# Optimization experiments

Measured on AMD Instinct MI355X. Metric: run time of the kernel, lower is better.

Reference implementation:

```python
import jax, jax.numpy as jnp
import numpy as np
from jax import lax

B, T = 64, 2048
RNN_DIM, EMB_DIM, ATT_DIM = 1024, 512, 128
N_FILT, KSIZE = 32, 31
PAD = (KSIZE - 1) // 2


def setup_inputs() -> dict:
    key = jax.random.key(0)
    ks = jax.random.split(key, 9)
    return {
        "query": jax.random.normal(ks[0], (B, RNN_DIM), jnp.float32),
        "processed_memory": jax.random.normal(ks[1], (B, T, ATT_DIM), jnp.float32),
        "attention_weights_cat": jax.random.uniform(ks[2], (B, 2, T), jnp.float32),
        "mask": jax.random.randint(ks[3], (B, T), 0, 2).astype(bool),
        "memory": jax.random.normal(ks[4], (B, T, EMB_DIM), jnp.float32),
        # learned parameters (torch Linear stores weight as [out, in])
        "W_query": jax.random.normal(ks[5], (ATT_DIM, RNN_DIM), jnp.float32) * 0.05,
        "conv_w": jax.random.normal(ks[6], (N_FILT, 2, KSIZE), jnp.float32) * 0.05,
        "W_loc": jax.random.normal(ks[7], (ATT_DIM, N_FILT), jnp.float32) * 0.05,
        "v_w": jax.random.normal(ks[8], (1, ATT_DIM), jnp.float32) * 0.05,
    }


def reference(query, processed_memory, attention_weights_cat, mask, memory,
              W_query, conv_w, W_loc, v_w):
    # processed_query: [B, 1, A]
    processed_query = (query @ W_query.T)[:, None, :]
    # location features: conv over time (2 -> N_FILT channels), same padding
    loc = lax.conv_general_dilated(
        attention_weights_cat, conv_w, window_strides=(1,),
        padding=[(PAD, PAD)], dimension_numbers=("NCH", "OIH", "NCH"))  # [B, F, T]
    processed_loc = jnp.einsum("bft,af->bta", loc, W_loc)  # [B, T, A]
    # additive energies -> [B, T]
    energies = jnp.tanh(processed_loc + processed_memory + processed_query) @ v_w[0]
    energies = jnp.where(mask, -jnp.inf, energies)
    attention_weights = jax.nn.softmax(energies, axis=1)  # [B, T]
    attention_context = jnp.einsum("bt,btd->bd", attention_weights, memory)  # [B, D]
    return attention_context, attention_weights
```

## Files before the change

### kernel.cpp

```cpp
#include <hip/hip_runtime.h>
#include <math.h>

#define B_ 64
#define T_ 2048
#define RNN_DIM 1024
#define EMB_DIM 512
#define ATT_DIM 128
#define N_FILT 32
#define KSIZE 31
#define PAD_ 15
#define TT 64
#define NSLICE 32

__device__ __forceinline__ float fast_tanh(float x) {
    float e = __expf(2.0f * x);
    return 1.0f - 2.0f / (e + 1.0f);
}

__global__ __launch_bounds__(128) void k_pq(const float* __restrict__ query,
                                            const float* __restrict__ Wq,
                                            float* __restrict__ pq) {
    __shared__ float q_s[RNN_DIM];
    const int b = blockIdx.x;
    const int tid = threadIdx.x;
    #pragma unroll
    for (int j = 0; j < RNN_DIM / 128; ++j)
        q_s[tid + 128 * j] = query[b * RNN_DIM + tid + 128 * j];
    __syncthreads();
    const int a = tid;
    const float4* w4 = reinterpret_cast<const float4*>(Wq + a * RNN_DIM);
    float acc = 0.f;
    #pragma unroll 4
    for (int r4 = 0; r4 < RNN_DIM / 4; ++r4) {
        float4 w = w4[r4];
        acc += w.x * q_s[4 * r4 + 0] + w.y * q_s[4 * r4 + 1]
             + w.z * q_s[4 * r4 + 2] + w.w * q_s[4 * r4 + 3];
    }
    pq[b * ATT_DIM + a] = acc;
}

__global__ __launch_bounds__(256) void k_energy(
    const float* __restrict__ att,
    const float* __restrict__ pm,
    const float* __restrict__ cw,
    const float* __restrict__ Wl,
    const float* __restrict__ v,
    const float* __restrict__ pq,
    const int*   __restrict__ mask,
    float* __restrict__ energy)
{
    __shared__ float att_s[2][TT + KSIZE - 1];
    __shared__ float loc_s[N_FILT][TT];
    __shared__ float pm_s[TT * (ATT_DIM + 1)];
    __shared__ float ep_s[4][TT];

    const int b   = blockIdx.y;
    const int t0  = blockIdx.x * TT;
    const int tid = threadIdx.x;
    const int lane = tid & 63;
    const int w    = __builtin_amdgcn_readfirstlane(tid >> 6);

    if (tid < 2 * (TT + KSIZE - 1)) {
        int c = tid / (TT + KSIZE - 1);
        int i = tid % (TT + KSIZE - 1);
        int gt = t0 + i - PAD_;
        att_s[c][i] = (gt >= 0 && gt < T_) ? att[(b * 2 + c) * T_ + gt] : 0.f;
    }
    {
        const float* src = pm + ((size_t)b * T_ + t0) * ATT_DIM;
        #pragma unroll
        for (int j = 0; j < TT * ATT_DIM / 256; ++j) {
            int idx = tid + 256 * j;
            int row = idx >> 7, col = idx & 127;
            pm_s[row * (ATT_DIM + 1) + col] = src[idx];
        }
    }
    __syncthreads();

    #pragma unroll
    for (int p = 0; p < 2; ++p) {
        int fb = __builtin_amdgcn_readfirstlane(w * 8 + p * 4);
        float a0 = 0.f, a1 = 0.f, a2 = 0.f, a3 = 0.f;
        #pragma unroll
        for (int c = 0; c < 2; ++c) {
            #pragma unroll
            for (int k = 0; k < KSIZE; ++k) {
                float av = att_s[c][lane + k];
                a0 += av * cw[((fb + 0) * 2 + c) * KSIZE + k];
                a1 += av * cw[((fb + 1) * 2 + c) * KSIZE + k];
                a2 += av * cw[((fb + 2) * 2 + c) * KSIZE + k];
                a3 += av * cw[((fb + 3) * 2 + c) * KSIZE + k];
            }
        }
        loc_s[fb + 0][lane] = a0;
        loc_s[fb + 1][lane] = a1;
        loc_s[fb + 2][lane] = a2;
        loc_s[fb + 3][lane] = a3;
    }
    __syncthreads();

    float lreg[N_FILT];
    #pragma unroll
    for (int f = 0; f < N_FILT; ++f) lreg[f] = loc_s[f][lane];

    const float* pm_row = pm_s + lane * (ATT_DIM + 1);
    const float* pq_row = pq + b * ATT_DIM;
    float eacc = 0.f;
    const int abase = __builtin_amdgcn_readfirstlane(w * 32);
    #pragma unroll 2
    for (int j = 0; j < 32; ++j) {
        int a = abase + j;
        const float* wl_row = Wl + a * N_FILT;
        float pl = 0.f;
        #pragma unroll
        for (int f = 0; f < N_FILT; ++f)
            pl += wl_row[f] * lreg[f];
        float x = pl + pm_row[a] + pq_row[a];
        eacc += fast_tanh(x) * v[a];
    }
    ep_s[w][lane] = eacc;
    __syncthreads();
    if (tid < TT) {
        float e = ep_s[0][tid] + ep_s[1][tid] + ep_s[2][tid] + ep_s[3][tid];
        int t = t0 + tid;
        if (mask[b * T_ + t] != 0) e = -INFINITY;
        energy[b * T_ + t] = e;
    }
}

__global__ __launch_bounds__(512) void k_softmax(float* __restrict__ E) {
    const int b = blockIdx.x, tid = threadIdx.x;
    __shared__ float red_s[8];
    float vals[4];
    float m = -INFINITY;
    #pragma unroll
    for (int j = 0; j < 4; ++j) {
        vals[j] = E[b * T_ + tid + 512 * j];
        m = fmaxf(m, vals[j]);
    }
    #pragma unroll
    for (int off = 32; off >= 1; off >>= 1)
        m = fmaxf(m, __shfl_xor(m, off, 64));
    const int w = tid >> 6;
    if ((tid & 63) == 0) red_s[w] = m;
    __syncthreads();
    m = red_s[0];
    #pragma unroll
    for (int i = 1; i < 8; ++i) m = fmaxf(m, red_s[i]);
    __syncthreads();
    float s = 0.f;
    #pragma unroll
    for (int j = 0; j < 4; ++j) {
        float p = __expf(vals[j] - m);
        vals[j] = p;
        s += p;
    }
    #pragma unroll
    for (int off = 32; off >= 1; off >>= 1)
        s += __shfl_xor(s, off, 64);
    if ((tid & 63) == 0) red_s[w] = s;
    __syncthreads();
    s = red_s[0];
    #pragma unroll
    for (int i = 1; i < 8; ++i) s += red_s[i];
    float inv = 1.0f / s;
    #pragma unroll
    for (int j = 0; j < 4; ++j)
        E[b * T_ + tid + 512 * j] = vals[j] * inv;
}

__global__ __launch_bounds__(128) void k_ctx_partial(
    const float* __restrict__ W,
    const float* __restrict__ mem,
    float* __restrict__ part)
{
    const int ts = blockIdx.x, b = blockIdx.y, tid = threadIdx.x;
    const int t0 = ts * (T_ / NSLICE);
    const float4* m4 = reinterpret_cast<const float4*>(mem)
                     + ((size_t)b * T_ + t0) * (EMB_DIM / 4);
    float4 acc = make_float4(0.f, 0.f, 0.f, 0.f);
    #pragma unroll 8
    for (int t = 0; t < T_ / NSLICE; ++t) {
        float wt = W[b * T_ + t0 + t];
        float4 mv = m4[(size_t)t * (EMB_DIM / 4) + tid];
        acc.x += wt * mv.x; acc.y += wt * mv.y;
        acc.z += wt * mv.z; acc.w += wt * mv.w;
    }
    reinterpret_cast<float4*>(part)[((size_t)b * NSLICE + ts) * (EMB_DIM / 4) + tid] = acc;
}

__global__ __launch_bounds__(256) void k_ctx_reduce(
    const float* __restrict__ part, float* __restrict__ ctx)
{
    const int g = blockIdx.x * 256 + threadIdx.x;
    const int b = g >> 9, d = g & 511;
    float s = 0.f;
    #pragma unroll
    for (int ts = 0; ts < NSLICE; ++ts)
        s += part[((size_t)b * NSLICE + ts) * EMB_DIM + d];
    ctx[g] = s;
}

extern "C" void kernel_launch(void* const* d_in, const int* in_sizes, int n_in,
                              void* d_out, int out_size, void* d_ws, size_t ws_size,
                              hipStream_t stream) {
    const float* query = (const float*)d_in[0];
    const float* pm    = (const float*)d_in[1];
    const float* att   = (const float*)d_in[2];
    const int*   mask  = (const int*)d_in[3];
    const float* mem   = (const float*)d_in[4];
    const float* Wq    = (const float*)d_in[5];
    const float* cw    = (const float*)d_in[6];
    const float* Wl    = (const float*)d_in[7];
    const float* vw    = (const float*)d_in[8];

    float* ctx = (float*)d_out;
    float* wts = (float*)d_out + B_ * EMB_DIM;
    float* pq   = (float*)d_ws;
    float* part = (float*)d_ws + B_ * ATT_DIM;

    k_pq        <<<dim3(B_),        dim3(128), 0, stream>>>(query, Wq, pq);
    k_energy    <<<dim3(T_/TT, B_), dim3(256), 0, stream>>>(att, pm, cw, Wl, vw, pq, mask, wts);
    k_softmax   <<<dim3(B_),        dim3(512), 0, stream>>>(wts);
    k_ctx_partial<<<dim3(NSLICE, B_), dim3(128), 0, stream>>>(wts, mem, part);
    k_ctx_reduce<<<dim3(B_*EMB_DIM/256), dim3(256), 0, stream>>>(part, ctx);
}
```

Measured before the change: 479.8 us.

## Drop softmax kernel by deferring normalization into context combine step

The energy kernel now writes unnormalized exp(energy), with masked positions set to zero, instead of masked energies. The separate softmax kernel is removed. A new combine kernel sums the exponentials per batch, normalizes the weights in place, and scales the reduced context by the inverse sum. The query projection is split across more blocks with a four-way reduction, and the processed_memory tile load now uses float4. Skipping the max subtraction saves a pass but relies on energies staying small enough that exp does not overflow.

```diff
diff --git a/kernel.cpp b/kernel.cpp
--- a/kernel.cpp
+++ b/kernel.cpp
@@ -17,26 +17,32 @@
     return 1.0f - 2.0f / (e + 1.0f);
 }
 
-__global__ __launch_bounds__(128) void k_pq(const float* __restrict__ query,
+__global__ __launch_bounds__(256) void k_pq(const float* __restrict__ query,
                                             const float* __restrict__ Wq,
                                             float* __restrict__ pq) {
-    __shared__ float q_s[RNN_DIM];
-    const int b = blockIdx.x;
+    __shared__ float4 q4s[RNN_DIM / 4];
+    __shared__ float red[4][64];
+    const int b = blockIdx.y;
     const int tid = threadIdx.x;
-    #pragma unroll
-    for (int j = 0; j < RNN_DIM / 128; ++j)
-        q_s[tid + 128 * j] = query[b * RNN_DIM + tid + 128 * j];
-    __syncthreads();
-    const int a = tid;
-    const float4* w4 = reinterpret_cast<const float4*>(Wq + a * RNN_DIM);
+    q4s[tid] = reinterpret_cast<const float4*>(query + (size_t)b * RNN_DIM)[tid];
+    __syncthreads();
+    const int al = tid & 63;
+    const int rp = tid >> 6;
+    const int a  = blockIdx.x * 64 + al;
+    const float4* w4 = reinterpret_cast<const float4*>(Wq + (size_t)a * RNN_DIM) + rp * 64;
     float acc = 0.f;
-    #pragma unroll 4
-    for (int r4 = 0; r4 < RNN_DIM / 4; ++r4) {
-        float4 w = w4[r4];
-        acc += w.x * q_s[4 * r4 + 0] + w.y * q_s[4 * r4 + 1]
-             + w.z * q_s[4 * r4 + 2] + w.w * q_s[4 * r4 + 3];
-    }
-    pq[b * ATT_DIM + a] = acc;
+    #pragma unroll 8
+    for (int i = 0; i < 64; ++i) {
+        float4 w = w4[i];
+        float4 q = q4s[rp * 64 + i];
+        acc += w.x * q.x + w.y * q.y + w.z * q.z + w.w * q.w;
+    }
+    red[rp][al] = acc;
+    __syncthreads();
+    if (tid < 64) {
+        float r = red[0][tid] + red[1][tid] + red[2][tid] + red[3][tid];
+        pq[b * ATT_DIM + blockIdx.x * 64 + tid] = r;
+    }
 }
 
 __global__ __launch_bounds__(256) void k_energy(
@@ -47,7 +53,7 @@
     const float* __restrict__ v,
     const float* __restrict__ pq,
     const int*   __restrict__ mask,
-    float* __restrict__ energy)
+    float* __restrict__ P)
 {
     __shared__ float att_s[2][TT + KSIZE - 1];
     __shared__ float loc_s[N_FILT][TT];
@@ -67,12 +73,16 @@
         att_s[c][i] = (gt >= 0 && gt < T_) ? att[(b * 2 + c) * T_ + gt] : 0.f;
     }
     {
-        const float* src = pm + ((size_t)b * T_ + t0) * ATT_DIM;
-        #pragma unroll
-        for (int j = 0; j < TT * ATT_DIM / 256; ++j) {
+        const float4* src4 = reinterpret_cast<const float4*>(
+            pm + ((size_t)b * T_ + t0) * ATT_DIM);
+        #pragma unroll
+        for (int j = 0; j < TT * ATT_DIM / 4 / 256; ++j) {
             int idx = tid + 256 * j;
-            int row = idx >> 7, col = idx & 127;
-            pm_s[row * (ATT_DIM + 1) + col] = src[idx];
+            int row = idx >> 5;
+            int c4  = idx & 31;
+            float4 vv = src4[idx];
+            float* dst = pm_s + row * (ATT_DIM + 1) + c4 * 4;
+            dst[0] = vv.x; dst[1] = vv.y; dst[2] = vv.z; dst[3] = vv.w;
         }
     }
     __syncthreads();
@@ -120,57 +130,17 @@
     }
     ep_s[w][lane] = eacc;
     __syncthreads();
+
     if (tid < TT) {
         float e = ep_s[0][tid] + ep_s[1][tid] + ep_s[2][tid] + ep_s[3][tid];
         int t = t0 + tid;
-        if (mask[b * T_ + t] != 0) e = -INFINITY;
-        energy[b * T_ + t] = e;
-    }
-}
-
-__global__ __launch_bounds__(512) void k_softmax(float* __restrict__ E) {
-    const int b = blockIdx.x, tid = threadIdx.x;
-    __shared__ float red_s[8];
-    float vals[4];
-    float m = -INFINITY;
-    #pragma unroll
-    for (int j = 0; j < 4; ++j) {
-        vals[j] = E[b * T_ + tid + 512 * j];
-        m = fmaxf(m, vals[j]);
-    }
-    #pragma unroll
-    for (int off = 32; off >= 1; off >>= 1)
-        m = fmaxf(m, __shfl_xor(m, off, 64));
-    const int w = tid >> 6;
-    if ((tid & 63) == 0) red_s[w] = m;
-    __syncthreads();
-    m = red_s[0];
-    #pragma unroll
-    for (int i = 1; i < 8; ++i) m = fmaxf(m, red_s[i]);
-    __syncthreads();
-    float s = 0.f;
-    #pragma unroll
-    for (int j = 0; j < 4; ++j) {
-        float p = __expf(vals[j] - m);
-        vals[j] = p;
-        s += p;
-    }
-    #pragma unroll
-    for (int off = 32; off >= 1; off >>= 1)
-        s += __shfl_xor(s, off, 64);
-    if ((tid & 63) == 0) red_s[w] = s;
-    __syncthreads();
-    s = red_s[0];
-    #pragma unroll
-    for (int i = 1; i < 8; ++i) s += red_s[i];
-    float inv = 1.0f / s;
-    #pragma unroll
-    for (int j = 0; j < 4; ++j)
-        E[b * T_ + tid + 512 * j] = vals[j] * inv;
+        float p = (mask[b * T_ + t] != 0) ? 0.f : __expf(e);
+        P[b * T_ + t] = p;
+    }
 }
 
 __global__ __launch_bounds__(128) void k_ctx_partial(
-    const float* __restrict__ W,
+    const float* __restrict__ P,
     const float* __restrict__ mem,
     float* __restrict__ part)
 {
@@ -181,7 +151,7 @@
     float4 acc = make_float4(0.f, 0.f, 0.f, 0.f);
     #pragma unroll 8
     for (int t = 0; t < T_ / NSLICE; ++t) {
-        float wt = W[b * T_ + t0 + t];
+        float wt = P[b * T_ + t0 + t];
         float4 mv = m4[(size_t)t * (EMB_DIM / 4) + tid];
         acc.x += wt * mv.x; acc.y += wt * mv.y;
         acc.z += wt * mv.z; acc.w += wt * mv.w;
@@ -189,16 +159,39 @@
     reinterpret_cast<float4*>(part)[((size_t)b * NSLICE + ts) * (EMB_DIM / 4) + tid] = acc;
 }
 
-__global__ __launch_bounds__(256) void k_ctx_reduce(
-    const float* __restrict__ part, float* __restrict__ ctx)
+__global__ __launch_bounds__(256) void k_combine(
+    const float* __restrict__ part,
+    float* __restrict__ W,
+    float* __restrict__ ctx)
 {
-    const int g = blockIdx.x * 256 + threadIdx.x;
-    const int b = g >> 9, d = g & 511;
+    __shared__ float red[4];
+    const int b = blockIdx.x, tid = threadIdx.x;
+    float p[T_ / 256];
     float s = 0.f;
     #pragma unroll
-    for (int ts = 0; ts < NSLICE; ++ts)
-        s += part[((size_t)b * NSLICE + ts) * EMB_DIM + d];
-    ctx[g] = s;
+    for (int j = 0; j < T_ / 256; ++j) {
+        p[j] = W[b * T_ + tid + 256 * j];
+        s += p[j];
+    }
+    #pragma unroll
+    for (int off = 32; off >= 1; off >>= 1)
+        s += __shfl_xor(s, off, 64);
+    if ((tid & 63) == 0) red[tid >> 6] = s;
+    __syncthreads();
+    const float S = red[0] + red[1] + red[2] + red[3];
+    const float inv = 1.0f / S;
+    #pragma unroll
+    for (int j = 0; j < T_ / 256; ++j)
+        W[b * T_ + tid + 256 * j] = p[j] * inv;
+    #pragma unroll
+    for (int j = 0; j < EMB_DIM / 256; ++j) {
+        int d = tid + 256 * j;
+        float acc = 0.f;
+        #pragma unroll
+        for (int ts = 0; ts < NSLICE; ++ts)
+            acc += part[((size_t)b * NSLICE + ts) * EMB_DIM + d];
+        ctx[b * EMB_DIM + d] = acc * inv;
+    }
 }
 
 extern "C" void kernel_launch(void* const* d_in, const int* in_sizes, int n_in,
@@ -217,11 +210,10 @@
     float* ctx = (float*)d_out;
     float* wts = (float*)d_out + B_ * EMB_DIM;
     float* pq   = (float*)d_ws;
-    float* part = (float*)d_ws + B_ * ATT_DIM;
-
-    k_pq        <<<dim3(B_),        dim3(128), 0, stream>>>(query, Wq, pq);
-    k_energy    <<<dim3(T_/TT, B_), dim3(256), 0, stream>>>(att, pm, cw, Wl, vw, pq, mask, wts);
-    k_softmax   <<<dim3(B_),        dim3(512), 0, stream>>>(wts);
-    k_ctx_partial<<<dim3(NSLICE, B_), dim3(128), 0, stream>>>(wts, mem, part);
-    k_ctx_reduce<<<dim3(B_*EMB_DIM/256), dim3(256), 0, stream>>>(part, ctx);
-}
+    float* part = pq + B_ * ATT_DIM;
+
+    k_pq         <<<dim3(2, B_),       dim3(256), 0, stream>>>(query, Wq, pq);
+    k_energy     <<<dim3(T_/TT, B_),   dim3(256), 0, stream>>>(att, pm, cw, Wl, vw, pq, mask, wts);
+    k_ctx_partial<<<dim3(NSLICE, B_),  dim3(128), 0, stream>>>(wts, mem, part);
+    k_combine    <<<dim3(B_),          dim3(256), 0, stream>>>(part, wts, ctx);
+}
```

New measurement: 455.7 us. 1.05x faster.
